# Optimization experiments

Hardware: AMD Instinct MI355X
Metric: run time of the kernel (lower is better)

## Reference

```python
import jax, jax.numpy as jnp
import numpy as np

N, IN_DIM, OUT_DIM, HEADS = 50000, 256, 256, 8
C = OUT_DIM // HEADS  # per-head channels = 32
E = 800000
G = 64  # number of graphs in the batch
NEG_SLOPE = 0.2
GN_EPS = 1e-5


def setup_inputs() -> dict:
    key = jax.random.key(0)
    ks = jax.random.split(key, 12)
    x = jax.random.normal(ks[0], (N, IN_DIM), dtype=jnp.float32)
    edge_index = jax.random.randint(ks[1], (2, E), 0, N, dtype=jnp.int64)
    batch = jnp.sort(jax.random.randint(ks[2], (N,), 0, G, dtype=jnp.int64))
    s = 1.0 / np.sqrt(IN_DIM)
    W_l = jax.random.uniform(ks[3], (IN_DIM, HEADS * C), jnp.float32, -s, s)
    b_l = jnp.zeros((HEADS * C,), jnp.float32)
    W_r = jax.random.uniform(ks[4], (IN_DIM, HEADS * C), jnp.float32, -s, s)
    b_r = jnp.zeros((HEADS * C,), jnp.float32)
    att = jax.random.normal(ks[5], (HEADS, C), dtype=jnp.float32) / np.sqrt(C)
    bias = jnp.zeros((HEADS * C,), jnp.float32)
    gn_weight = jnp.ones((OUT_DIM,), jnp.float32)
    gn_bias = jnp.zeros((OUT_DIM,), jnp.float32)
    gn_mean_scale = jnp.ones((OUT_DIM,), jnp.float32)
    return {"x": x, "edge_index": edge_index, "batch": batch,
            "W_l": W_l, "b_l": b_l, "W_r": W_r, "b_r": b_r,
            "att": att, "bias": bias, "gn_weight": gn_weight,
            "gn_bias": gn_bias, "gn_mean_scale": gn_mean_scale}


def _gat_block(x, src, dst, batch, W_l, b_l, W_r, b_r, att, bias,
               gn_weight, gn_bias, gn_mean_scale):
    n = x.shape[0]
    # GATv2Conv (add_self_loops=True, concat=True)
    loops = jnp.arange(n, dtype=src.dtype)
    src = jnp.concatenate([src, loops])
    dst = jnp.concatenate([dst, loops])
    xl = (x @ W_l + b_l).reshape(n, HEADS, C)  # source transform
    xr = (x @ W_r + b_r).reshape(n, HEADS, C)  # target transform
    e = jax.nn.leaky_relu(xl[src] + xr[dst], NEG_SLOPE)  # [E', H, C]
    logits = jnp.einsum('ehc,hc->eh', e, att)            # [E', H]
    # segment softmax over incoming edges of each destination node
    m = jax.ops.segment_max(logits, dst, num_segments=n)
    alpha = jnp.exp(logits - m[dst])
    denom = jax.ops.segment_sum(alpha, dst, num_segments=n)
    alpha = alpha / (denom[dst] + 1e-16)
    msg = xl[src] * alpha[:, :, None]                    # [E', H, C]
    h = jax.ops.segment_sum(msg, dst, num_segments=n).reshape(n, HEADS * C) + bias
    # identity residual (in_dim == out_dim) + ELU
    h = jax.nn.elu(h + x)
    # GraphNorm (post-norm)
    counts = jnp.maximum(jax.ops.segment_sum(jnp.ones((n,), h.dtype), batch,
                                             num_segments=G), 1.0)
    mean = jax.ops.segment_sum(h, batch, num_segments=G) / counts[:, None]
    out0 = h - gn_mean_scale * mean[batch]
    var = jax.ops.segment_sum(out0 * out0, batch, num_segments=G) / counts[:, None]
    return gn_weight * out0 / jnp.sqrt(var[batch] + GN_EPS) + gn_bias


def reference(x, edge_index, batch, W_l, b_l, W_r, b_r, att, bias,
              gn_weight, gn_bias, gn_mean_scale):
    return _gat_block(x, edge_index[0], edge_index[1], batch,
                      W_l, b_l, W_r, b_r, att, bias,
                      gn_weight, gn_bias, gn_mean_scale)
```

## Files before the change

kernel.cpp:

```cpp
#include <hip/hip_runtime.h>
#include <hip/hip_bf16.h>
#include <stdint.h>

#define N_NODES 50000
#define MPAD    50048
#define IN_DIM  256
#define EDGES   800000
#define EPRIME  (EDGES + N_NODES)
#define NGRAPH  64
#define GN_EPS  1e-5f
#define ECPAD   53248
#define NBLK    208

typedef __attribute__((ext_vector_type(8))) short short8;
typedef __attribute__((ext_vector_type(4))) float floatx4;
typedef __attribute__((ext_vector_type(2))) float float2v;

__device__ __forceinline__ uint32_t pk2bf(float a, float b) {
    union { __hip_bfloat162 h; uint32_t u; } cv;
    cv.h = __float22bfloat162_rn(make_float2(a, b));
    return cv.u;
}

__device__ __forceinline__ unsigned short f2b(float f) {
    uint32_t u = __float_as_uint(f);
    u += 0x7fffu + ((u >> 16) & 1u);
    return (unsigned short)(u >> 16);
}

__global__ __launch_bounds__(256) void k_prep_w(const float* __restrict__ Wl,
                                                const float* __restrict__ Wr,
                                                unsigned short* __restrict__ Wt) {
    int idx = blockIdx.x * 256 + threadIdx.x;
    int n = idx >> 8, k = idx & 255;
    float v = (n < 256) ? Wl[k * 256 + n] : Wr[k * 256 + (n - 256)];
    Wt[idx] = f2b(v);
}

__global__ __launch_bounds__(512) void k_gemm(const float* __restrict__ x,
                                              const unsigned short* __restrict__ Wt,
                                              const float* __restrict__ bl,
                                              const float* __restrict__ br,
                                              unsigned short* __restrict__ XL,
                                              unsigned short* __restrict__ XR) {
    __shared__ unsigned short As[64 * 256];
    int rbase = blockIdx.x * 64;
    int tid = threadIdx.x;

#pragma unroll
    for (int it = 0; it < 4; ++it) {
        int c = it * 512 + tid;
        int row = c >> 5, ch = c & 31;
        int gr = rbase + row;
        float4 f0, f1;
        if (gr < N_NODES) {
            const float4* src = (const float4*)(x + (size_t)gr * 256 + ch * 8);
            f0 = src[0]; f1 = src[1];
        } else {
            f0 = make_float4(0.f,0.f,0.f,0.f); f1 = f0;
        }
        uint32_t p0 = pk2bf(f0.x, f0.y), p1 = pk2bf(f0.z, f0.w);
        uint32_t p2 = pk2bf(f1.x, f1.y), p3 = pk2bf(f1.z, f1.w);
        uint4 hv = make_uint4(p0, p1, p2, p3);
        *(uint4*)(As + row * 256 + (ch ^ (row & 7)) * 8) = hv;
    }
    __syncthreads();

    int w = tid >> 6;
    int l = tid & 63;
    int m = l & 15, q = l >> 4;

    floatx4 acc[4][4];
#pragma unroll
    for (int rf = 0; rf < 4; ++rf)
#pragma unroll
        for (int cf = 0; cf < 4; ++cf)
            acc[rf][cf] = (floatx4){0.f, 0.f, 0.f, 0.f};

    const unsigned short* wbase = Wt + (size_t)(w * 64) * 256;

#pragma unroll
    for (int kk = 0; kk < 8; ++kk) {
        short8 a[4];
#pragma unroll
        for (int rf = 0; rf < 4; ++rf) {
            int row = rf * 16 + m;
            int ch = (kk * 4 + q) ^ (row & 7);
            a[rf] = *(const short8*)(As + row * 256 + ch * 8);
        }
#pragma unroll
        for (int cf = 0; cf < 4; ++cf) {
            short8 b = *(const short8*)(wbase + (size_t)(cf * 16 + m) * 256 + kk * 32 + q * 8);
#pragma unroll
            for (int rf = 0; rf < 4; ++rf)
                acc[rf][cf] = __builtin_amdgcn_mfma_f32_16x16x32_bf16(b, a[rf], acc[rf][cf], 0, 0, 0);
        }
    }

    unsigned short* obase = (w < 4) ? XL : XR;
    const float* bptr = (w < 4) ? bl : br;
    int cb = (w & 3) * 64;
#pragma unroll
    for (int cf = 0; cf < 4; ++cf) {
        int chb = cb + cf * 16 + q * 4;
        float4 bv = *(const float4*)(bptr + chb);
#pragma unroll
        for (int rf = 0; rf < 4; ++rf) {
            int node = rbase + rf * 16 + m;
            uint2 o;
            o.x = pk2bf(acc[rf][cf][0] + bv.x, acc[rf][cf][1] + bv.y);
            o.y = pk2bf(acc[rf][cf][2] + bv.z, acc[rf][cf][3] + bv.w);
            *(uint2*)(obase + (size_t)node * 256 + chb) = o;
        }
    }
}

__global__ __launch_bounds__(256) void k_hist(const int* __restrict__ ei,
                                              const int* __restrict__ batch,
                                              int* __restrict__ ecount,
                                              int* __restrict__ ncount,
                                              int* __restrict__ sedge) {
    __shared__ int hist[NGRAPH];
    if (threadIdx.x < NGRAPH) hist[threadIdx.x] = 0;
    __syncthreads();
    int e = blockIdx.x * 256 + threadIdx.x;
    if (e < EPRIME) {
        int d = (e < EDGES) ? ei[EDGES + e] : (e - EDGES);
        atomicAdd(&ecount[d], 1);
    }
    if (e < N_NODES) atomicAdd(&hist[batch[e]], 1);
    if (blockIdx.x == 0 && threadIdx.x < 16) sedge[EPRIME + threadIdx.x] = 0;
    __syncthreads();
    if (threadIdx.x < NGRAPH && hist[threadIdx.x])
        atomicAdd(&ncount[threadIdx.x], hist[threadIdx.x]);
}

__global__ __launch_bounds__(256) void k_scan1(const int* __restrict__ ecount,
                                               int* __restrict__ bsum) {
    __shared__ int red[256];
    int v = ecount[blockIdx.x * 256 + threadIdx.x];
    red[threadIdx.x] = v;
    __syncthreads();
    for (int off = 128; off > 0; off >>= 1) {
        if (threadIdx.x < off) red[threadIdx.x] += red[threadIdx.x + off];
        __syncthreads();
    }
    if (threadIdx.x == 0) bsum[blockIdx.x] = red[0];
}

__global__ __launch_bounds__(256) void k_scan2(int* __restrict__ bsum) {
    __shared__ int buf[256];
    int t = threadIdx.x;
    int v = (t < NBLK) ? bsum[t] : 0;
    buf[t] = v;
    __syncthreads();
    for (int off = 1; off < 256; off <<= 1) {
        int p = (t >= off) ? buf[t - off] : 0;
        __syncthreads();
        buf[t] += p;
        __syncthreads();
    }
    if (t < NBLK) bsum[t] = buf[t] - v;
}

__global__ __launch_bounds__(256) void k_scan3(const int* __restrict__ ecount,
                                               const int* __restrict__ bsum,
                                               int* __restrict__ estart,
                                               int* __restrict__ ecursor) {
    __shared__ int buf[256];
    int b = blockIdx.x, t = threadIdx.x;
    int v = ecount[b * 256 + t];
    buf[t] = v;
    __syncthreads();
    for (int off = 1; off < 256; off <<= 1) {
        int p = (t >= off) ? buf[t - off] : 0;
        __syncthreads();
        buf[t] += p;
        __syncthreads();
    }
    int e = bsum[b] + buf[t] - v;
    estart[b * 256 + t]  = e;
    ecursor[b * 256 + t] = e;
}

__global__ __launch_bounds__(256) void k_scatter(const int* __restrict__ ei,
                                                 int* __restrict__ ecursor,
                                                 int* __restrict__ sedge) {
    int e = blockIdx.x * 256 + threadIdx.x;
    if (e >= EPRIME) return;
    int s, d;
    if (e < EDGES) { s = ei[e]; d = ei[EDGES + e]; }
    else           { s = d = e - EDGES; }
    int pos = atomicAdd(&ecursor[d], 1);
    sedge[pos] = s;
}

__global__ __launch_bounds__(256) void k_msg(const unsigned short* __restrict__ XL,
                                             const unsigned short* __restrict__ XRb,
                                             const float* __restrict__ x,
                                             const float* __restrict__ att,
                                             const float* __restrict__ bias,
                                             const int* __restrict__ sedge,
                                             const int* __restrict__ estart,
                                             const int* __restrict__ ecount,
                                             float* __restrict__ out) {
    int d = (int)((blockIdx.x * 256 + threadIdx.x) >> 6);
    int l = threadIdx.x & 63;
    int lofs = l * 8;

    float4 xin  = ((const float4*)(x + (size_t)d * 256))[l];
    float4 bvv  = ((const float4*)bias)[l];
    float4 attv = ((const float4*)att)[l];
    float2v att01 = {attv.x, attv.y}, att23 = {attv.z, attv.w};

    uint2 xru = ((const uint2*)(XRb + (size_t)d * 256))[l];
    float2v xr01, xr23;
    xr01[0] = __uint_as_float(xru.x << 16);
    xr01[1] = __uint_as_float(xru.x & 0xffff0000u);
    xr23[0] = __uint_as_float(xru.y << 16);
    xr23[1] = __uint_as_float(xru.y & 0xffff0000u);

    int s0  = __builtin_amdgcn_readfirstlane(estart[d]);
    int cnt = __builtin_amdgcn_readfirstlane(ecount[d]);

    auto ldrow = [&](int src) -> uint2 {
        size_t off = ((size_t)(uint32_t)__builtin_amdgcn_readfirstlane(src)) << 9;
        return *(const uint2*)((const char*)XL + off + lofs);
    };

    float den0 = 0.f, den1 = 0.f, den2 = 0.f, den3 = 0.f;
    float2v A01 = {0.f,0.f}, A23 = {0.f,0.f};
    float2v B01 = {0.f,0.f}, B23 = {0.f,0.f};
    float2v C01 = {0.f,0.f}, C23 = {0.f,0.f};
    float2v D01 = {0.f,0.f}, D23 = {0.f,0.f};

    auto proc = [&](uint2 U, float& den, float2v& R01, float2v& R23) {
        float2v x01, x23;
        x01[0] = __uint_as_float(U.x << 16);
        x01[1] = __uint_as_float(U.x & 0xffff0000u);
        x23[0] = __uint_as_float(U.y << 16);
        x23[1] = __uint_as_float(U.y & 0xffff0000u);
        float2v e01 = x01 + xr01, e23 = x23 + xr23;
        float2v f01 = e01 * 0.2f, f23 = e23 * 0.2f;
        e01[0] = fmaxf(e01[0], f01[0]); e01[1] = fmaxf(e01[1], f01[1]);
        e23[0] = fmaxf(e23[0], f23[0]); e23[1] = fmaxf(e23[1], f23[1]);
        float2v pp2 = e01 * att01 + e23 * att23;
        float pp = pp2[0] + pp2[1];
        {
            int pi = __float_as_int(pp);
            pp += __int_as_float(__builtin_amdgcn_update_dpp(0, pi, 0xB1, 0xF, 0xF, true));
            pi = __float_as_int(pp);
            pp += __int_as_float(__builtin_amdgcn_update_dpp(0, pi, 0x4E, 0xF, 0xF, true));
            pp += __int_as_float(__builtin_amdgcn_ds_swizzle(__float_as_int(pp), 0x101F));
        }
        float al = __expf(fminf(pp, 80.f));
        den += al;
        float2v al2 = {al, al};
        R01 += al2 * x01;
        R23 += al2 * x23;
    };

    uint2 P0 = ldrow(sedge[s0]);
    uint2 P1 = ldrow(sedge[s0 + 1]);
    uint2 P2 = ldrow(sedge[s0 + 2]);
    uint2 P3 = ldrow(sedge[s0 + 3]);

    int nq = cnt >> 2;
    for (int qq = 0; qq < nq; ++qq) {
        uint2 Q0 = P0, Q1 = P1, Q2 = P2, Q3 = P3;
        int nb = s0 + (qq + 1) * 4;
        P0 = ldrow(sedge[nb]);
        P1 = ldrow(sedge[nb + 1]);
        P2 = ldrow(sedge[nb + 2]);
        P3 = ldrow(sedge[nb + 3]);
        proc(Q0, den0, A01, A23);
        proc(Q1, den1, B01, B23);
        proc(Q2, den2, C01, C23);
        proc(Q3, den3, D01, D23);
    }
    int rem = cnt & 3;
    if (rem > 0) proc(P0, den0, A01, A23);
    if (rem > 1) proc(P1, den1, B01, B23);
    if (rem > 2) proc(P2, den2, C01, C23);

    float inv = 1.f / ((den0 + den1) + (den2 + den3) + 1e-16f);
    A01 = (A01 + B01) + (C01 + D01);
    A23 = (A23 + B23) + (C23 + D23);

    float h0 = A01[0] * inv + bvv.x + xin.x; h0 = (h0 > 0.f) ? h0 : (__expf(h0) - 1.f);
    float h1 = A01[1] * inv + bvv.y + xin.y; h1 = (h1 > 0.f) ? h1 : (__expf(h1) - 1.f);
    float h2 = A23[0] * inv + bvv.z + xin.z; h2 = (h2 > 0.f) ? h2 : (__expf(h2) - 1.f);
    float h3 = A23[1] * inv + bvv.w + xin.w; h3 = (h3 > 0.f) ? h3 : (__expf(h3) - 1.f);
    ((float4*)(out + (size_t)d * 256))[l] = make_float4(h0, h1, h2, h3);
}

#define GN_ROWS 64
__global__ __launch_bounds__(256) void k_gn_sum(const float* __restrict__ h,
                                                const int* __restrict__ batch,
                                                float* __restrict__ gsum,
                                                float* __restrict__ gsq) {
    __shared__ int bsh[GN_ROWS];
    int r0 = blockIdx.x * GN_ROWS;
    if (threadIdx.x < GN_ROWS) {
        int i = r0 + threadIdx.x;
        bsh[threadIdx.x] = (i < N_NODES) ? batch[i] : -1;
    }
    __syncthreads();
    int c = threadIdx.x;
    float s1 = 0.f, s2 = 0.f;
    int g = bsh[0];
    for (int j = 0; j < GN_ROWS; j += 4) {
        int i = r0 + j;
        if (i >= N_NODES) break;
        bool full = (i + 3 < N_NODES);
        if (full && bsh[j] == g && bsh[j + 3] == g) {
            const float* hp = h + (size_t)i * 256 + c;
            float v0 = hp[0], v1 = hp[256], v2 = hp[512], v3 = hp[768];
            s1 += (v0 + v1) + (v2 + v3);
            s2 += (v0 * v0 + v1 * v1) + (v2 * v2 + v3 * v3);
        } else {
            for (int jj = j; jj < j + 4; ++jj) {
                int ii = r0 + jj;
                if (ii >= N_NODES) break;
                int bg = bsh[jj];
                if (bg != g) {
                    atomicAdd(&gsum[g * 256 + c], s1);
                    atomicAdd(&gsq[g * 256 + c], s2);
                    s1 = 0.f; s2 = 0.f; g = bg;
                }
                float v = h[(size_t)ii * 256 + c];
                s1 += v; s2 += v * v;
            }
        }
    }
    atomicAdd(&gsum[g * 256 + c], s1);
    atomicAdd(&gsq[g * 256 + c], s2);
}

__global__ __launch_bounds__(256) void k_final(float* __restrict__ out,
                                               const int* __restrict__ batch,
                                               const float* __restrict__ gsum,
                                               const float* __restrict__ gsq,
                                               const int* __restrict__ ncount,
                                               const float* __restrict__ gnw,
                                               const float* __restrict__ gnb,
                                               const float* __restrict__ gms) {
    int idx = blockIdx.x * 256 + threadIdx.x;
    int i = idx >> 6, l = idx & 63;
    if (i >= N_NODES) return;
    int g = batch[i];
    float inv = 1.f / fmaxf((float)ncount[g], 1.f);
    float4 hv = ((const float4*)(out + (size_t)i * 256))[l];
    float4 ms = ((const float4*)(gsum + g * 256))[l];
    float4 qs = ((const float4*)(gsq  + g * 256))[l];
    float4 wv = ((const float4*)gnw)[l];
    float4 bv = ((const float4*)gnb)[l];
    float4 sv = ((const float4*)gms)[l];
    float4 o;
    {
        float m = ms.x * inv, q = qs.x * inv;
        o.x = wv.x * (hv.x - sv.x * m) * rsqrtf(q - m * m * sv.x * (2.f - sv.x) + GN_EPS) + bv.x;
    }
    {
        float m = ms.y * inv, q = qs.y * inv;
        o.y = wv.y * (hv.y - sv.y * m) * rsqrtf(q - m * m * sv.y * (2.f - sv.y) + GN_EPS) + bv.y;
    }
    {
        float m = ms.z * inv, q = qs.z * inv;
        o.z = wv.z * (hv.z - sv.z * m) * rsqrtf(q - m * m * sv.z * (2.f - sv.z) + GN_EPS) + bv.z;
    }
    {
        float m = ms.w * inv, q = qs.w * inv;
        o.w = wv.w * (hv.w - sv.w * m) * rsqrtf(q - m * m * sv.w * (2.f - sv.w) + GN_EPS) + bv.w;
    }
    ((float4*)(out + (size_t)i * 256))[l] = o;
}

extern "C" void kernel_launch(void* const* d_in, const int* in_sizes, int n_in,
                              void* d_out, int out_size, void* d_ws, size_t ws_size,
                              hipStream_t stream) {
    const float* x    = (const float*)d_in[0];
    const int*   ei   = (const int*)d_in[1];
    const int*   batch= (const int*)d_in[2];
    const float* Wl   = (const float*)d_in[3];
    const float* bl   = (const float*)d_in[4];
    const float* Wr   = (const float*)d_in[5];
    const float* br   = (const float*)d_in[6];
    const float* att  = (const float*)d_in[7];
    const float* bias = (const float*)d_in[8];
    const float* gnw  = (const float*)d_in[9];
    const float* gnb  = (const float*)d_in[10];
    const float* gms  = (const float*)d_in[11];
    float* out = (float*)d_out;

    char* p = (char*)d_ws;
    auto alloc = [&](size_t bytes) -> char* {
        char* r = p;
        p += (bytes + 255) & ~(size_t)255;
        return r;
    };
    unsigned short* Wt  = (unsigned short*)alloc((size_t)512 * 256 * 2);
    unsigned short* XL  = (unsigned short*)alloc((size_t)MPAD * 256 * 2);
    unsigned short* XRb = (unsigned short*)alloc((size_t)MPAD * 256 * 2);
    int* estart         = (int*)alloc((size_t)ECPAD * 4);
    int* ecursor        = (int*)alloc((size_t)ECPAD * 4);
    int* sedge          = (int*)alloc((size_t)(EPRIME + 16) * 4);
    int* bsum           = (int*)alloc((size_t)256 * 4);
    int* ecount         = (int*)alloc((size_t)ECPAD * 4);
    int* ncount         = (int*)alloc((size_t)NGRAPH * 4);
    float* gsum         = (float*)alloc((size_t)2 * NGRAPH * 256 * 4);
    float* gsq          = gsum + NGRAPH * 256;
    size_t zbytes = (size_t)((char*)(gsum + 2 * NGRAPH * 256) - (char*)ecount);
    hipMemsetAsync(ecount, 0, zbytes, stream);

    k_prep_w<<<512, 256, 0, stream>>>(Wl, Wr, Wt);
    k_gemm<<<MPAD / 64, 512, 0, stream>>>(x, Wt, bl, br, XL, XRb);

    k_hist<<<(EPRIME + 255) / 256, 256, 0, stream>>>(ei, batch, ecount, ncount, sedge);
    k_scan1<<<NBLK, 256, 0, stream>>>(ecount, bsum);
    k_scan2<<<1, 256, 0, stream>>>(bsum);
    k_scan3<<<NBLK, 256, 0, stream>>>(ecount, bsum, estart, ecursor);
    k_scatter<<<(EPRIME + 255) / 256, 256, 0, stream>>>(ei, ecursor, sedge);

    k_msg<<<N_NODES / 4, 256, 0, stream>>>(XL, XRb, x, att, bias,
                                           sedge, estart, ecount, out);

    k_gn_sum<<<(N_NODES + GN_ROWS - 1) / GN_ROWS, 256, 0, stream>>>(out, batch, gsum, gsq);
    k_final<<<N_NODES * 64 / 256, 256, 0, stream>>>(out, batch, gsum, gsq,
                                                    ncount, gnw, gnb, gms);
}
```

Measured before the change: 364.4 us.

## Fuse GraphNorm stats into message kernel, single-block scan, preload edge sources

Merges the three-kernel prefix scan into one 1024-thread single-block scan. The GraphNorm sum and sum-of-squares pass moves into the message kernel as per-node atomics. Edge source indices are preloaded into registers and broadcast with readlane. Leaky ReLU is rewritten algebraically as 0.6*z + 0.4*|z| with att folded in. This saves launches and one full pass over h, at the cost of heavy float atomic contention on 64 graph rows (8 atomics per lane per node) and a serial scan on one block.

After: 964.8 us. 165% more time.

```diff
diff --git a/kernel.cpp b/kernel.cpp
--- a/kernel.cpp
+++ b/kernel.cpp
@@ -26,6 +26,13 @@
     uint32_t u = __float_as_uint(f);
     u += 0x7fffu + ((u >> 16) & 1u);
     return (unsigned short)(u >> 16);
+}
+
+__device__ __forceinline__ float2v up2(uint32_t u) {
+    float2v r;
+    r[0] = __uint_as_float(u << 16);
+    r[1] = __uint_as_float(u & 0xffff0000u);
+    return r;
 }
 
 __global__ __launch_bounds__(256) void k_prep_w(const float* __restrict__ Wl,
@@ -129,58 +136,44 @@
         atomicAdd(&ecount[d], 1);
     }
     if (e < N_NODES) atomicAdd(&hist[batch[e]], 1);
-    if (blockIdx.x == 0 && threadIdx.x < 16) sedge[EPRIME + threadIdx.x] = 0;
+    if (blockIdx.x == 0 && threadIdx.x < 192) sedge[EPRIME + threadIdx.x] = 0;
     __syncthreads();
     if (threadIdx.x < NGRAPH && hist[threadIdx.x])
         atomicAdd(&ncount[threadIdx.x], hist[threadIdx.x]);
 }
 
-__global__ __launch_bounds__(256) void k_scan1(const int* __restrict__ ecount,
-                                               int* __restrict__ bsum) {
-    __shared__ int red[256];
-    int v = ecount[blockIdx.x * 256 + threadIdx.x];
-    red[threadIdx.x] = v;
-    __syncthreads();
-    for (int off = 128; off > 0; off >>= 1) {
-        if (threadIdx.x < off) red[threadIdx.x] += red[threadIdx.x + off];
+__global__ __launch_bounds__(1024) void k_scan_all(const int* __restrict__ ecount,
+                                                   int* __restrict__ estart,
+                                                   int* __restrict__ ecursor) {
+    __shared__ int wsum[16];
+    int t = threadIdx.x, w = t >> 6, l = t & 63;
+    int carry = 0;
+    for (int base = 0; base < ECPAD; base += 4096) {
+        int4 v = ((const int4*)(ecount + base))[t];
+        int s = v.x + v.y + v.z + v.w;
+        int sc = s;
+#pragma unroll
+        for (int off = 1; off < 64; off <<= 1) {
+            int n = __shfl_up(sc, off);
+            sc += (l >= off) ? n : 0;
+        }
+        if (l == 63) wsum[w] = sc;
         __syncthreads();
-    }
-    if (threadIdx.x == 0) bsum[blockIdx.x] = red[0];
-}
-
-__global__ __launch_bounds__(256) void k_scan2(int* __restrict__ bsum) {
-    __shared__ int buf[256];
-    int t = threadIdx.x;
-    int v = (t < NBLK) ? bsum[t] : 0;
-    buf[t] = v;
-    __syncthreads();
-    for (int off = 1; off < 256; off <<= 1) {
-        int p = (t >= off) ? buf[t - off] : 0;
+        int woff = 0, ctot = 0;
+#pragma unroll
+        for (int i = 0; i < 16; ++i) {
+            int wi = wsum[i];
+            woff += (i < w) ? wi : 0;
+            ctot += wi;
+        }
+        int e0 = carry + woff + (sc - s);
+        int4 o;
+        o.x = e0; o.y = e0 + v.x; o.z = o.y + v.y; o.w = o.z + v.z;
+        ((int4*)(estart  + base))[t] = o;
+        ((int4*)(ecursor + base))[t] = o;
+        carry += ctot;
         __syncthreads();
-        buf[t] += p;
-        __syncthreads();
-    }
-    if (t < NBLK) bsum[t] = buf[t] - v;
-}
-
-__global__ __launch_bounds__(256) void k_scan3(const int* __restrict__ ecount,
-                                               const int* __restrict__ bsum,
-                                               int* __restrict__ estart,
-                                               int* __restrict__ ecursor) {
-    __shared__ int buf[256];
-    int b = blockIdx.x, t = threadIdx.x;
-    int v = ecount[b * 256 + t];
-    buf[t] = v;
-    __syncthreads();
-    for (int off = 1; off < 256; off <<= 1) {
-        int p = (t >= off) ? buf[t - off] : 0;
-        __syncthreads();
-        buf[t] += p;
-        __syncthreads();
-    }
-    int e = bsum[b] + buf[t] - v;
-    estart[b * 256 + t]  = e;
-    ecursor[b * 256 + t] = e;
+    }
 }
 
 __global__ __launch_bounds__(256) void k_scatter(const int* __restrict__ ei,
@@ -200,10 +193,12 @@
                                              const float* __restrict__ x,
                                              const float* __restrict__ att,
                                              const float* __restrict__ bias,
+                                             const int* __restrict__ batch,
                                              const int* __restrict__ sedge,
                                              const int* __restrict__ estart,
                                              const int* __restrict__ ecount,
-                                             float* __restrict__ out) {
+                                             float* __restrict__ out,
+                                             float* __restrict__ gsum) {
     int d = (int)((blockIdx.x * 256 + threadIdx.x) >> 6);
     int l = threadIdx.x & 63;
     int lofs = l * 8;
@@ -211,18 +206,32 @@
     float4 xin  = ((const float4*)(x + (size_t)d * 256))[l];
     float4 bvv  = ((const float4*)bias)[l];
     float4 attv = ((const float4*)att)[l];
-    float2v att01 = {attv.x, attv.y}, att23 = {attv.z, attv.w};
+    float2v a601 = {0.6f * attv.x, 0.6f * attv.y};
+    float2v a623 = {0.6f * attv.z, 0.6f * attv.w};
+    float a40 = 0.4f * attv.x, a41 = 0.4f * attv.y;
+    float a42 = 0.4f * attv.z, a43 = 0.4f * attv.w;
 
     uint2 xru = ((const uint2*)(XRb + (size_t)d * 256))[l];
-    float2v xr01, xr23;
-    xr01[0] = __uint_as_float(xru.x << 16);
-    xr01[1] = __uint_as_float(xru.x & 0xffff0000u);
-    xr23[0] = __uint_as_float(xru.y << 16);
-    xr23[1] = __uint_as_float(xru.y & 0xffff0000u);
+    float2v xr01 = up2(xru.x), xr23 = up2(xru.y);
 
     int s0  = __builtin_amdgcn_readfirstlane(estart[d]);
     int cnt = __builtin_amdgcn_readfirstlane(ecount[d]);
-
+    int g   = __builtin_amdgcn_readfirstlane(batch[d]);
+
+    int esrc0 = sedge[s0 + l];
+    int esrc1 = sedge[s0 + 64 + l];
+
+    auto getsrc = [&](int i) -> int {
+        int r;
+        if (i < 128) {
+            int lo = __builtin_amdgcn_readlane(esrc0, i & 63);
+            int hi = __builtin_amdgcn_readlane(esrc1, i & 63);
+            r = (i < 64) ? lo : hi;
+        } else {
+            r = sedge[s0 + i];
+        }
+        return r;
+    };
     auto ldrow = [&](int src) -> uint2 {
         size_t off = ((size_t)(uint32_t)__builtin_amdgcn_readfirstlane(src)) << 9;
         return *(const uint2*)((const char*)XL + off + lofs);
@@ -235,24 +244,20 @@
     float2v D01 = {0.f,0.f}, D23 = {0.f,0.f};
 
     auto proc = [&](uint2 U, float& den, float2v& R01, float2v& R23) {
-        float2v x01, x23;
-        x01[0] = __uint_as_float(U.x << 16);
-        x01[1] = __uint_as_float(U.x & 0xffff0000u);
-        x23[0] = __uint_as_float(U.y << 16);
-        x23[1] = __uint_as_float(U.y & 0xffff0000u);
-        float2v e01 = x01 + xr01, e23 = x23 + xr23;
-        float2v f01 = e01 * 0.2f, f23 = e23 * 0.2f;
-        e01[0] = fmaxf(e01[0], f01[0]); e01[1] = fmaxf(e01[1], f01[1]);
-        e23[0] = fmaxf(e23[0], f23[0]); e23[1] = fmaxf(e23[1], f23[1]);
-        float2v pp2 = e01 * att01 + e23 * att23;
-        float pp = pp2[0] + pp2[1];
-        {
-            int pi = __float_as_int(pp);
-            pp += __int_as_float(__builtin_amdgcn_update_dpp(0, pi, 0xB1, 0xF, 0xF, true));
-            pi = __float_as_int(pp);
-            pp += __int_as_float(__builtin_amdgcn_update_dpp(0, pi, 0x4E, 0xF, 0xF, true));
-            pp += __int_as_float(__builtin_amdgcn_ds_swizzle(__float_as_int(pp), 0x101F));
-        }
+        float2v x01 = up2(U.x), x23 = up2(U.y);
+        float2v z01 = x01 + xr01, z23 = x23 + xr23;
+        float2v q = z01 * a601 + z23 * a623;
+        float t0 = fmaf(fabsf(z01[0]), a40, q[0]);
+        float t1 = fmaf(fabsf(z01[1]), a41, q[1]);
+        t0 = fmaf(fabsf(z23[0]), a42, t0);
+        t1 = fmaf(fabsf(z23[1]), a43, t1);
+        float pp = t0 + t1;
+        int pi = __float_as_int(pp);
+        pp += __int_as_float(__builtin_amdgcn_update_dpp(0, pi, 0xB1, 0xF, 0xF, true));
+        pi = __float_as_int(pp);
+        pp += __int_as_float(__builtin_amdgcn_update_dpp(0, pi, 0x4E, 0xF, 0xF, true));
+        pi = __float_as_int(pp);
+        pp += __int_as_float(__builtin_amdgcn_update_dpp(0, pi, 0x141, 0xF, 0xF, true));
         float al = __expf(fminf(pp, 80.f));
         den += al;
         float2v al2 = {al, al};
@@ -260,19 +265,19 @@
         R23 += al2 * x23;
     };
 
-    uint2 P0 = ldrow(sedge[s0]);
-    uint2 P1 = ldrow(sedge[s0 + 1]);
-    uint2 P2 = ldrow(sedge[s0 + 2]);
-    uint2 P3 = ldrow(sedge[s0 + 3]);
+    uint2 P0 = ldrow(getsrc(0));
+    uint2 P1 = ldrow(getsrc(1));
+    uint2 P2 = ldrow(getsrc(2));
+    uint2 P3 = ldrow(getsrc(3));
 
     int nq = cnt >> 2;
     for (int qq = 0; qq < nq; ++qq) {
         uint2 Q0 = P0, Q1 = P1, Q2 = P2, Q3 = P3;
-        int nb = s0 + (qq + 1) * 4;
-        P0 = ldrow(sedge[nb]);
-        P1 = ldrow(sedge[nb + 1]);
-        P2 = ldrow(sedge[nb + 2]);
-        P3 = ldrow(sedge[nb + 3]);
+        int nb = (qq + 1) * 4;
+        P0 = ldrow(getsrc(nb));
+        P1 = ldrow(getsrc(nb + 1));
+        P2 = ldrow(getsrc(nb + 2));
+        P3 = ldrow(getsrc(nb + 3));
         proc(Q0, den0, A01, A23);
         proc(Q1, den1, B01, B23);
         proc(Q2, den2, C01, C23);
@@ -292,49 +297,17 @@
     float h2 = A23[0] * inv + bvv.z + xin.z; h2 = (h2 > 0.f) ? h2 : (__expf(h2) - 1.f);
     float h3 = A23[1] * inv + bvv.w + xin.w; h3 = (h3 > 0.f) ? h3 : (__expf(h3) - 1.f);
     ((float4*)(out + (size_t)d * 256))[l] = make_float4(h0, h1, h2, h3);
-}
-
-#define GN_ROWS 64
-__global__ __launch_bounds__(256) void k_gn_sum(const float* __restrict__ h,
-                                                const int* __restrict__ batch,
-                                                float* __restrict__ gsum,
-                                                float* __restrict__ gsq) {
-    __shared__ int bsh[GN_ROWS];
-    int r0 = blockIdx.x * GN_ROWS;
-    if (threadIdx.x < GN_ROWS) {
-        int i = r0 + threadIdx.x;
-        bsh[threadIdx.x] = (i < N_NODES) ? batch[i] : -1;
-    }
-    __syncthreads();
-    int c = threadIdx.x;
-    float s1 = 0.f, s2 = 0.f;
-    int g = bsh[0];
-    for (int j = 0; j < GN_ROWS; j += 4) {
-        int i = r0 + j;
-        if (i >= N_NODES) break;
-        bool full = (i + 3 < N_NODES);
-        if (full && bsh[j] == g && bsh[j + 3] == g) {
-            const float* hp = h + (size_t)i * 256 + c;
-            float v0 = hp[0], v1 = hp[256], v2 = hp[512], v3 = hp[768];
-            s1 += (v0 + v1) + (v2 + v3);
-            s2 += (v0 * v0 + v1 * v1) + (v2 * v2 + v3 * v3);
-        } else {
-            for (int jj = j; jj < j + 4; ++jj) {
-                int ii = r0 + jj;
-                if (ii >= N_NODES) break;
-                int bg = bsh[jj];
-                if (bg != g) {
-                    atomicAdd(&gsum[g * 256 + c], s1);
-                    atomicAdd(&gsq[g * 256 + c], s2);
-                    s1 = 0.f; s2 = 0.f; g = bg;
-                }
-                float v = h[(size_t)ii * 256 + c];
-                s1 += v; s2 += v * v;
-            }
-        }
-    }
-    atomicAdd(&gsum[g * 256 + c], s1);
-    atomicAdd(&gsq[g * 256 + c], s2);
+
+    float* gsp = gsum + (size_t)g * 256 + 4 * l;
+    atomicAdd(gsp + 0, h0);
+    atomicAdd(gsp + 1, h1);
+    atomicAdd(gsp + 2, h2);
+    atomicAdd(gsp + 3, h3);
+    float* gqp = gsp + NGRAPH * 256;
+    atomicAdd(gqp + 0, h0 * h0);
+    atomicAdd(gqp + 1, h1 * h1);
+    atomicAdd(gqp + 2, h2 * h2);
+    atomicAdd(gqp + 3, h3 * h3);
 }
 
 __global__ __launch_bounds__(256) void k_final(float* __restrict__ out,
@@ -404,8 +377,7 @@
     unsigned short* XRb = (unsigned short*)alloc((size_t)MPAD * 256 * 2);
     int* estart         = (int*)alloc((size_t)ECPAD * 4);
     int* ecursor        = (int*)alloc((size_t)ECPAD * 4);
-    int* sedge          = (int*)alloc((size_t)(EPRIME + 16) * 4);
-    int* bsum           = (int*)alloc((size_t)256 * 4);
+    int* sedge          = (int*)alloc((size_t)(EPRIME + 192) * 4);
     int* ecount         = (int*)alloc((size_t)ECPAD * 4);
     int* ncount         = (int*)alloc((size_t)NGRAPH * 4);
     float* gsum         = (float*)alloc((size_t)2 * NGRAPH * 256 * 4);
@@ -417,15 +389,12 @@
     k_gemm<<<MPAD / 64, 512, 0, stream>>>(x, Wt, bl, br, XL, XRb);
 
     k_hist<<<(EPRIME + 255) / 256, 256, 0, stream>>>(ei, batch, ecount, ncount, sedge);
-    k_scan1<<<NBLK, 256, 0, stream>>>(ecount, bsum);
-    k_scan2<<<1, 256, 0, stream>>>(bsum);
-    k_scan3<<<NBLK, 256, 0, stream>>>(ecount, bsum, estart, ecursor);
+    k_scan_all<<<1, 1024, 0, stream>>>(ecount, estart, ecursor);
     k_scatter<<<(EPRIME + 255) / 256, 256, 0, stream>>>(ei, ecursor, sedge);
 
-    k_msg<<<N_NODES / 4, 256, 0, stream>>>(XL, XRb, x, att, bias,
-                                           sedge, estart, ecount, out);
-
-    k_gn_sum<<<(N_NODES + GN_ROWS - 1) / GN_ROWS, 256, 0, stream>>>(out, batch, gsum, gsq);
+    k_msg<<<N_NODES / 4, 256, 0, stream>>>(XL, XRb, x, att, bias, batch,
+                                           sedge, estart, ecount, out, gsum);
+
     k_final<<<N_NODES * 64 / 256, 256, 0, stream>>>(out, batch, gsum, gsq,
                                                     ncount, gnw, gnb, gms);
 }
```
